# Kernel optimization log

Measured on AMD Instinct MI355X. Metric: run time of the kernel, lower is better.

The kernel has to match this reference:

```python
import jax, jax.numpy as jnp
import numpy as np


def setup_inputs() -> dict:
    key = jax.random.key(0)
    k1, k2, k3 = jax.random.split(key, 3)
    n_way, n_shot, d, n_query = 5, 10, 1024, 16384
    n_support = n_way * n_shot
    train_imgs = jax.random.normal(k1, (n_support, d), dtype=jnp.float32)
    # one-hot labels: exactly n_shot examples per class (interleaved)
    cls = jnp.tile(jnp.arange(n_way), n_shot)  # [n_support]
    train_labels = jax.nn.one_hot(cls, n_way, dtype=jnp.int64)
    query_imgs = jax.random.normal(k2, (n_query, d), dtype=jnp.float32)
    query_labels = jax.random.randint(k3, (n_query,), 0, n_way)
    return {"train_imgs": train_imgs, "train_labels": train_labels,
            "query_imgs": query_imgs, "query_labels": query_labels}


def reference(train_imgs, train_labels, query_imgs, query_labels):
    # backbone = identity: imgs are already feature embeddings
    n_support, n_way = train_labels.shape
    n_shot = n_support // n_way  # static
    support = train_imgs                      # [n_support, d]
    query = query_imgs                        # [n_query, d]

    # group support features by class: [n_way, n_shot, d]
    cls = jnp.argmax(train_labels, axis=1)
    order = jnp.argsort(cls, stable=True)
    grouped = support[order].reshape(n_way, n_shot, -1)
    mats = jnp.swapaxes(grouped, 1, 2)        # [n_way, d, n_shot]

    # batched reduced SVD (torch.svd some=True -> full_matrices=False)
    U, _, _ = jnp.linalg.svd(mats, full_matrices=False)  # [n_way, d, n_shot]
    Uk = U[:, :, : n_shot - 1]                # [n_way, d, k]

    # projection of queries onto each class subspace: P = Uk Uk^T q
    coeff = jnp.einsum('wdk,qd->wkq', Uk, query)   # [n_way, k, n_query]
    proj = jnp.einsum('wdk,wkq->wqd', Uk, coeff)   # [n_way, n_query, d]
    dist = jnp.sum((query[None, :, :] - proj) ** 2, axis=-1)  # [n_way, n_query]

    logits = -dist.T                           # [n_query, n_way]
    # normalize=False in this configuration
    return jax.nn.log_softmax(logits, axis=1)
```

## Files before the change

### kernel.cpp

```cpp
#include <hip/hip_runtime.h>
#include <stdint.h>


typedef __attribute__((ext_vector_type(4))) float f32x4;
typedef __attribute__((ext_vector_type(8))) short s16x8;

#define WS_G_OFF    0
#define WS_GH_OFF   4096
#define WS_P_OFF    8192

#define RDL(x, l) __uint_as_float(__builtin_amdgcn_readlane(__float_as_uint(x), (l)))

__device__ __forceinline__ unsigned short f2bf(float f) {
  unsigned int u = __float_as_uint(f);
  u += 0x7FFFu + ((u >> 16) & 1u);
  return (unsigned short)(u >> 16);
}

__device__ __forceinline__ bool labels_int64(const int* L) {
  int cnt = 0; bool oddz = true;
  #pragma unroll
  for (int t = 0; t < 20; ++t) {
    int v = L[t];
    if (t & 1) { if (v) oddz = false; }
    else       { if (v) cnt++; }
  }
  return oddz && (cnt == 2);
}

__device__ __forceinline__ int cls_of(const int* L, bool is64, int i) {
  int best = -0x7fffffff, c = 0;
  #pragma unroll
  for (int j = 0; j < 5; ++j) {
    int v = is64 ? L[i * 10 + 2 * j] : L[i * 5 + j];
    if (v > best) { best = v; c = j; }
  }
  return c;
}

__global__ __launch_bounds__(256) void dsn_prep(const float* __restrict__ support,
                                                const int* __restrict__ labels,
                                                double* __restrict__ G,
                                                unsigned short* __restrict__ P) {
  int b = blockIdx.x;
  bool is64 = labels_int64(labels);

  if (b < 69) {
    int wid  = b * 4 + (threadIdx.x >> 6);
    int lane = threadIdx.x & 63;
    if (wid >= 275) return;
    int w = wid / 55, p = wid % 55;
    int a = 0;
    while (p >= 10 - a) { p -= 10 - a; a++; }
    int bb = a + p;

    int myc = (lane < 50) ? cls_of(labels, is64, lane) : -1;
    unsigned long long mask = __ballot(lane < 50 && myc == w);

    unsigned long long m = mask;
    for (int i = 0; i < a; ++i) m &= m - 1;
    int ia = __ffsll((unsigned long long)m) - 1;
    m = mask;
    for (int i = 0; i < bb; ++i) m &= m - 1;
    int ib = __ffsll((unsigned long long)m) - 1;

    const float* A = support + ia * 1024;
    const float* B = support + ib * 1024;
    double acc = 0.0;
    #pragma unroll
    for (int i = 0; i < 16; ++i) {
      int d = lane + 64 * i;
      acc += (double)A[d] * (double)B[d];
    }
    #pragma unroll
    for (int off = 32; off > 0; off >>= 1) acc += __shfl_xor(acc, off);
    if (lane == 0) {
      G[(w * 10 + a) * 10 + bb] = acc;
      G[(w * 10 + bb) * 10 + a] = acc;
    }
  } else {
    int r = b - 69;
    int w = r >> 4, kk = r & 15;
    int t = threadIdx.x;
    unsigned short* Prow = P + r * 1024;
    if (kk >= 10) {
      #pragma unroll
      for (int j = 0; j < 4; ++j) Prow[t + 256 * j] = 0;
      return;
    }
    __shared__ int sid;
    if (t < 64) {
      int myc = (t < 50) ? cls_of(labels, is64, t) : -1;
      unsigned long long mask = __ballot(t < 50 && myc == w);
      if (t == 0) {
        unsigned long long m = mask;
        for (int z = 0; z < kk; ++z) m &= m - 1;
        sid = __ffsll(m) - 1;
      }
    }
    __syncthreads();
    const float* src = support + (size_t)sid * 1024;
    #pragma unroll
    for (int j = 0; j < 4; ++j) Prow[t + 256 * j] = f2bf(src[t + 256 * j]);
  }
}

__global__ __launch_bounds__(64) void dsn_solve(const double* __restrict__ G,
                                                float* __restrict__ Ghat) {
  int w = blockIdx.x;
  int li = threadIdx.x;
  int rr = (li < 10) ? li : 0;
  const double* Gr = G + w * 100 + rr * 10;

  float o[10], g[10], h[10];
  #pragma unroll
  for (int j = 0; j < 10; ++j) {
    o[j] = (float)Gr[j];
    g[j] = o[j];
    h[j] = (li == j) ? 1.f : 0.f;
  }

  #pragma unroll
  for (int k = 0; k < 10; ++k) {
    float piv = 1.f / RDL(g[k], k);
    float pg[10], ph[10];
    #pragma unroll
    for (int j = 0; j < 10; ++j) {
      pg[j] = RDL(g[j], k) * piv;
      ph[j] = RDL(h[j], k) * piv;
    }
    float f = g[k];
    bool isk = (li == k);
    #pragma unroll
    for (int j = 0; j < 10; ++j) {
      g[j] = isk ? pg[j] : g[j] - f * pg[j];
      h[j] = isk ? ph[j] : h[j] - f * ph[j];
    }
  }

  float b[10];
  float d = h[0];
  #pragma unroll
  for (int k = 1; k < 10; ++k) d = (li == k) ? h[k] : d;
  float dm = RDL(d, 0);
  #pragma unroll
  for (int k = 1; k < 10; ++k) dm = fmaxf(dm, RDL(d, k));
  float rn = 1.f / dm;
  #pragma unroll
  for (int j = 0; j < 10; ++j) b[j] = h[j] * rn;
  float db = d * rn;

  int jmx = 0;
  float bv = RDL(db, 0);
  float trB = bv;
  #pragma unroll
  for (int k = 1; k < 10; ++k) {
    float t2 = RDL(db, k);
    trB += t2;
    if (t2 > bv) { bv = t2; jmx = k; }
  }
  float sigma = (trB - bv) * (1.f / 9.f);
  sigma = fminf(fmaxf(sigma, 0.f), 0.92f);
  float rs = 1.f / (bv - sigma);

  float x = (li == jmx) ? 1.f : 0.f;
  #pragma unroll
  for (int it = 0; it < 16; ++it) {
    float xn = 0.f;
    #pragma unroll
    for (int k = 0; k < 10; ++k) xn += b[k] * RDL(x, k);
    x = rs * (xn - sigma * x);
  }
  #pragma unroll
  for (int it = 0; it < 2; ++it) {
    float xn = 0.f;
    #pragma unroll
    for (int k = 0; k < 10; ++k) xn += b[k] * RDL(x, k);
    float ax = fabsf(xn);
    float mx = RDL(ax, 0);
    #pragma unroll
    for (int k = 1; k < 10; ++k) mx = fmaxf(mx, RDL(ax, k));
    x = xn * (1.f / mx);
  }
  float v = x;

  float gv = 0.f;
  #pragma unroll
  for (int k = 0; k < 10; ++k) gv += o[k] * RDL(v, k);
  float tn = v * gv;
  float denom = RDL(tn, 0);
  #pragma unroll
  for (int k = 1; k < 10; ++k) denom += RDL(tn, k);
  float rden = 1.f / denom;
  if (li < 10) {
    #pragma unroll
    for (int j = 0; j < 10; ++j)
      Ghat[w * 100 + li * 10 + j] = h[j] - v * RDL(v, j) * rden;
  }
}

__global__ __launch_bounds__(256, 4) void dsn_main(const float* __restrict__ query,
                                                   const unsigned short* __restrict__ P,
                                                   const float* __restrict__ Ghat,
                                                   float* __restrict__ out) {
  __shared__ float Zsh[4][80][17];
  __shared__ float Ghs[500];

  int t    = threadIdx.x;
  int wave = t >> 6;
  int lane = t & 63;
  int q0   = blockIdx.x * 16;
  int qrow = lane & 15;
  int kbase = wave * 256 + (lane >> 4) * 8;

  if (t < 250) {
    Ghs[t]       = Ghat[t];
    Ghs[t + 250] = Ghat[t + 250];
  }

  const float* qp = query + (size_t)(q0 + qrow) * 1024 + kbase;
  const unsigned short* up = P + qrow * 1024 + kbase;

  f32x4 acc[5];
  #pragma unroll
  for (int w = 0; w < 5; ++w) acc[w] = (f32x4){0.f, 0.f, 0.f, 0.f};

  #pragma unroll
  for (int kt = 0; kt < 8; ++kt) {
    const float* qk = qp + kt * 32;
    f32x4 lo = *(const f32x4*)qk;
    f32x4 hi = *(const f32x4*)(qk + 4);
    s16x8 bf;
    bf[0] = (short)f2bf(lo[0]); bf[1] = (short)f2bf(lo[1]);
    bf[2] = (short)f2bf(lo[2]); bf[3] = (short)f2bf(lo[3]);
    bf[4] = (short)f2bf(hi[0]); bf[5] = (short)f2bf(hi[1]);
    bf[6] = (short)f2bf(hi[2]); bf[7] = (short)f2bf(hi[3]);
    const unsigned short* uk = up + kt * 32;
    #pragma unroll
    for (int w = 0; w < 5; ++w) {
      s16x8 av = *(const s16x8*)(uk + w * 16384);
      acc[w] = __builtin_amdgcn_mfma_f32_16x16x32_bf16(av, bf, acc[w], 0, 0, 0);
    }
  }

  int rowbase = (lane >> 4) * 4;
  #pragma unroll
  for (int w = 0; w < 5; ++w) {
    #pragma unroll
    for (int r = 0; r < 4; ++r)
      Zsh[wave][w * 16 + rowbase + r][qrow] = acc[w][r];
  }
  __syncthreads();

  if (t < 16) {
    int q = q0 + t;
    float zv[50];
    #pragma unroll
    for (int w = 0; w < 5; ++w) {
      #pragma unroll
      for (int s = 0; s < 10; ++s) {
        float z = Zsh[0][w * 16 + s][t];
        #pragma unroll
        for (int sp = 1; sp < 4; ++sp) z += Zsh[sp][w * 16 + s][t];
        zv[w * 10 + s] = z;
      }
    }
    float sv[5];
    #pragma unroll
    for (int w = 0; w < 5; ++w) {
      float s = 0.f;
      #pragma unroll
      for (int i = 0; i < 10; ++i) {
        float gz = 0.f;
        #pragma unroll
        for (int j = 0; j < 10; ++j) gz += Ghs[w * 100 + i * 10 + j] * zv[w * 10 + j];
        s += zv[w * 10 + i] * gz;
      }
      sv[w] = s;
    }
    float mx = fmaxf(fmaxf(fmaxf(sv[0], sv[1]), fmaxf(sv[2], sv[3])), sv[4]);
    float sum = 0.f;
    #pragma unroll
    for (int w = 0; w < 5; ++w) sum += expf(sv[w] - mx);
    float lse = mx + logf(sum);
    float* o = out + (size_t)q * 5;
    #pragma unroll
    for (int w = 0; w < 5; ++w) o[w] = sv[w] - lse;
  }
}

extern "C" void kernel_launch(void* const* d_in, const int* in_sizes, int n_in,
                              void* d_out, int out_size, void* d_ws, size_t ws_size,
                              hipStream_t stream) {
  const float* support = (const float*)d_in[0];
  const int*   labels  = (const int*)d_in[1];
  const float* query   = (const float*)d_in[2];
  float* out = (float*)d_out;
  char* ws = (char*)d_ws;

  double*         G    = (double*)(ws + WS_G_OFF);
  float*          Ghat = (float*)(ws + WS_GH_OFF);
  unsigned short* P    = (unsigned short*)(ws + WS_P_OFF);

  int nq = in_sizes[2] / 1024;
  int main_blocks = nq / 16;

  hipLaunchKernelGGL(dsn_prep,  dim3(149), dim3(256), 0, stream, support, labels, G, P);
  hipLaunchKernelGGL(dsn_solve, dim3(5),   dim3(64),  0, stream, G, Ghat);
  hipLaunchKernelGGL(dsn_main,  dim3(main_blocks), dim3(256), 0, stream,
                     query, P, Ghat, out);
}
```

Baseline: 47.51 us.

## Stage query tile into LDS via async global_load_lds and preload P fragments

The query tile is now copied straight into a 64KB LDS buffer with global_load_lds, using an XOR swizzle so the later reads avoid bank conflicts. It is then read from LDS for the bf16 conversion instead of being loaded strided from global memory. All P fragments (40 vectors) are loaded into registers up front so their latency overlaps the async copy. Zsh and Ghat now share the same LDS buffer. In exchange, register pressure goes up and the large LDS footprint limits occupancy, and launch_bounds no longer asks for 4 blocks.

```diff
diff --git a/kernel.cpp b/kernel.cpp
--- a/kernel.cpp
+++ b/kernel.cpp
@@ -15,6 +15,12 @@
   unsigned int u = __float_as_uint(f);
   u += 0x7FFFu + ((u >> 16) & 1u);
   return (unsigned short)(u >> 16);
+}
+
+__device__ __forceinline__ void gld_lds16(const float* g, float* l) {
+  __builtin_amdgcn_global_load_lds(
+      (const __attribute__((address_space(1))) float*)g,
+      (__attribute__((address_space(3))) float*)l, 16, 0, 0);
 }
 
 __device__ __forceinline__ bool labels_int64(const int* L) {
@@ -199,57 +205,69 @@
   }
 }
 
-__global__ __launch_bounds__(256, 4) void dsn_main(const float* __restrict__ query,
-                                                   const unsigned short* __restrict__ P,
-                                                   const float* __restrict__ Ghat,
-                                                   float* __restrict__ out) {
-  __shared__ float Zsh[4][80][17];
-  __shared__ float Ghs[500];
+__global__ __launch_bounds__(256) void dsn_main(const float* __restrict__ query,
+                                                const unsigned short* __restrict__ P,
+                                                const float* __restrict__ Ghat,
+                                                float* __restrict__ out) {
+  __shared__ float smem[16384];
 
   int t    = threadIdx.x;
   int wave = t >> 6;
   int lane = t & 63;
   int q0   = blockIdx.x * 16;
   int qrow = lane & 15;
-  int kbase = wave * 256 + (lane >> 4) * 8;
-
-  if (t < 250) {
-    Ghs[t]       = Ghat[t];
-    Ghs[t + 250] = Ghat[t + 250];
-  }
-
-  const float* qp = query + (size_t)(q0 + qrow) * 1024 + kbase;
-  const unsigned short* up = P + qrow * 1024 + kbase;
-
+  int g    = lane >> 4;
+
+  #pragma unroll
+  for (int i = 0; i < 16; ++i) {
+    int c = wave * 16 + i;
+    int r = c >> 2;
+    int u = (((c & 3) << 6) | lane) ^ ((r & 7) << 1);
+    gld_lds16(query + (size_t)(q0 + r) * 1024 + u * 4, smem + c * 256);
+  }
+
+  const unsigned short* up = P + qrow * 1024 + wave * 256 + g * 8;
+  s16x8 pv[8][5];
+  #pragma unroll
+  for (int kt = 0; kt < 8; ++kt)
+    #pragma unroll
+    for (int w = 0; w < 5; ++w)
+      pv[kt][w] = *(const s16x8*)(up + w * 16384 + kt * 32);
+  asm volatile("" ::: "memory");
+
+  __syncthreads();
+
+  int sw = (qrow & 7) << 1;
   f32x4 acc[5];
   #pragma unroll
   for (int w = 0; w < 5; ++w) acc[w] = (f32x4){0.f, 0.f, 0.f, 0.f};
 
   #pragma unroll
   for (int kt = 0; kt < 8; ++kt) {
-    const float* qk = qp + kt * 32;
-    f32x4 lo = *(const f32x4*)qk;
-    f32x4 hi = *(const f32x4*)(qk + 4);
+    int u0 = wave * 64 + g * 2 + kt * 8;
+    int fi = (qrow * 256 + (u0 ^ sw)) * 4;
+    f32x4 lo = *(const f32x4*)(smem + fi);
+    f32x4 hi = *(const f32x4*)(smem + fi + 4);
     s16x8 bf;
     bf[0] = (short)f2bf(lo[0]); bf[1] = (short)f2bf(lo[1]);
     bf[2] = (short)f2bf(lo[2]); bf[3] = (short)f2bf(lo[3]);
     bf[4] = (short)f2bf(hi[0]); bf[5] = (short)f2bf(hi[1]);
     bf[6] = (short)f2bf(hi[2]); bf[7] = (short)f2bf(hi[3]);
-    const unsigned short* uk = up + kt * 32;
-    #pragma unroll
-    for (int w = 0; w < 5; ++w) {
-      s16x8 av = *(const s16x8*)(uk + w * 16384);
-      acc[w] = __builtin_amdgcn_mfma_f32_16x16x32_bf16(av, bf, acc[w], 0, 0, 0);
-    }
-  }
-
-  int rowbase = (lane >> 4) * 4;
+    #pragma unroll
+    for (int w = 0; w < 5; ++w)
+      acc[w] = __builtin_amdgcn_mfma_f32_16x16x32_bf16(pv[kt][w], bf,
+                                                       acc[w], 0, 0, 0);
+  }
+  __syncthreads();
+
+  int rowbase = g * 4;
   #pragma unroll
   for (int w = 0; w < 5; ++w) {
     #pragma unroll
     for (int r = 0; r < 4; ++r)
-      Zsh[wave][w * 16 + rowbase + r][qrow] = acc[w][r];
-  }
+      smem[wave * 1360 + (w * 16 + rowbase + r) * 17 + qrow] = acc[w][r];
+  }
+  for (int i = t; i < 500; i += 256) smem[5440 + i] = Ghat[i];
   __syncthreads();
 
   if (t < 16) {
@@ -259,9 +277,10 @@
     for (int w = 0; w < 5; ++w) {
       #pragma unroll
       for (int s = 0; s < 10; ++s) {
-        float z = Zsh[0][w * 16 + s][t];
+        float z = smem[(w * 16 + s) * 17 + t];
         #pragma unroll
-        for (int sp = 1; sp < 4; ++sp) z += Zsh[sp][w * 16 + s][t];
+        for (int sp = 1; sp < 4; ++sp)
+          z += smem[sp * 1360 + (w * 16 + s) * 17 + t];
         zv[w * 10 + s] = z;
       }
     }
@@ -273,7 +292,8 @@
       for (int i = 0; i < 10; ++i) {
         float gz = 0.f;
         #pragma unroll
-        for (int j = 0; j < 10; ++j) gz += Ghs[w * 100 + i * 10 + j] * zv[w * 10 + j];
+        for (int j = 0; j < 10; ++j)
+          gz += smem[5440 + w * 100 + i * 10 + j] * zv[w * 10 + j];
         s += zv[w * 10 + i] * gz;
       }
       sv[w] = s;
```

After: 62.81 us. 32.2% more time.
